# Performance work log

Measured on AMD Instinct MI355X. Metric: run time of the kernel, lower is better.

Reference implementation:

```python
import jax, jax.numpy as jnp
import numpy as np

DIM = 1024
NUM_HEADS = 16
HEAD_DIM = DIM // NUM_HEADS


def apply_rotary_embed(x, thetas):
    # x: (..., seq, d), thetas: (seq, d) broadcast over leading dims
    x1, x2 = jnp.split(x, 2, axis=-1)
    x_rot = jnp.concatenate([-x2, x1], axis=-1)
    return x * jnp.cos(thetas) + x_rot * jnp.sin(thetas)


def setup_inputs() -> dict:
    key = jax.random.key(0)
    ks = jax.random.split(key, 8)
    B, Nx, Nc = 4, 1024, 2048
    x = jax.random.normal(ks[0], (B, Nx, DIM), dtype=jnp.float32)
    c = jax.random.normal(ks[1], (B, Nc, DIM), dtype=jnp.float32)
    x_pos_embed = jax.random.normal(ks[2], (Nx, HEAD_DIM), dtype=jnp.float32)
    c_pos_embed = jax.random.normal(ks[3], (Nc, HEAD_DIM), dtype=jnp.float32)
    s = 1.0 / np.sqrt(DIM)
    Wq = jax.random.normal(ks[4], (DIM, DIM), dtype=jnp.float32) * s
    Wkv = jax.random.normal(ks[5], (DIM, 2 * DIM), dtype=jnp.float32) * s
    Wproj = jax.random.normal(ks[6], (DIM, DIM), dtype=jnp.float32) * s
    bproj = jnp.zeros((DIM,), dtype=jnp.float32)
    return {"x": x, "c": c, "x_pos_embed": x_pos_embed, "c_pos_embed": c_pos_embed,
            "Wq": Wq, "Wkv": Wkv, "Wproj": Wproj, "bproj": bproj}


def reference(x, c, x_pos_embed, c_pos_embed, Wq, Wkv, Wproj, bproj):
    B, Nx, D = x.shape
    Nc = c.shape[1]
    H, hd = NUM_HEADS, HEAD_DIM
    # Q projection -> (B, H, Nx, hd)
    q = (x @ Wq).reshape(B, Nx, H, hd).transpose(0, 2, 1, 3)
    q = apply_rotary_embed(q, x_pos_embed)
    # KV projection -> k, v each (B, H, Nc, hd)
    kv = (c @ Wkv).reshape(B, Nc, 2, H, hd).transpose(2, 0, 3, 1, 4)
    k, v = kv[0], kv[1]
    k = apply_rotary_embed(k, c_pos_embed)
    # scaled dot-product attention (dropout p=0 -> identity)
    scale = 1.0 / np.sqrt(hd).astype(np.float32)
    attn = jnp.einsum('bhqd,bhkd->bhqk', q, k) * scale
    attn = jax.nn.softmax(attn, axis=-1)
    out = jnp.einsum('bhqk,bhkd->bhqd', attn, v)
    out = out.transpose(0, 2, 1, 3).reshape(B, Nx, D)
    return out @ Wproj + bproj
```

## Files before the change

kernel.cpp:

```cpp
#include <hip/hip_runtime.h>
#include <math.h>

#define DIMC  1024
#define NHEAD 16
#define HD    64
#define NB    4
#define NX    1024
#define NC    2048
#define KD    1024

typedef _Float16 half_t;
typedef __attribute__((ext_vector_type(8))) _Float16 h8;
typedef __attribute__((ext_vector_type(4))) _Float16 h4;
typedef __attribute__((ext_vector_type(2))) __fp16 fp16x2;
typedef __attribute__((ext_vector_type(4))) float f32x4;

#define QSCALE 0.1803368801111244f
#define NEGM  -8.656170245333781f

__device__ __forceinline__ void gload_lds16(const half_t* g, half_t* l) {
    __builtin_amdgcn_global_load_lds(
        (__attribute__((address_space(1))) void*)(g),
        (__attribute__((address_space(3))) void*)(l), 16, 0, 0);
}

__device__ __forceinline__ void wtile(const float* __restrict__ W,
                                      half_t* __restrict__ Wt, int N, int IMG,
                                      int bx, int by, int t)
{
    __shared__ half_t T[64][72];
    const int k0 = by * 64, n0 = bx * 64;
    const int kr = t >> 2, c0 = (t & 3) << 4;
    const float* src = W + (size_t)(k0 + kr) * N + n0 + c0;
#pragma unroll
    for (int j = 0; j < 16; j += 4) {
        float4 v = *(const float4*)(src + j);
        T[c0 + j + 0][kr] = (half_t)v.x;
        T[c0 + j + 1][kr] = (half_t)v.y;
        T[c0 + j + 2][kr] = (half_t)v.z;
        T[c0 + j + 3][kr] = (half_t)v.w;
    }
    __syncthreads();
    const int nr = t >> 2, kc = (t & 3) << 4;
    if (!IMG) {
        half_t* dst = Wt + (size_t)(n0 + nr) * KD + k0 + kc;
        *(int4*)dst       = *(const int4*)&T[nr][kc];
        *(int4*)(dst + 8) = *(const int4*)&T[nr][kc + 8];
    } else {
        const int n = n0 + nr;
        const int ntile = n >> 8, rr = n & 255;
        const int s0 = kc >> 3;
        half_t* base = Wt + ((size_t)(ntile * 16 + by) * 256 + rr) * 64;
        *(int4*)(base + ((s0 ^ (rr & 7)) << 3))       = *(const int4*)&T[nr][kc];
        *(int4*)(base + (((s0 + 1) ^ (rr & 7)) << 3)) = *(const int4*)&T[nr][kc + 8];
    }
}

__global__ __launch_bounds__(256) void prep(
    const float* __restrict__ x, half_t* __restrict__ xh,
    const float* __restrict__ c, half_t* __restrict__ ch,
    const float* __restrict__ xpe, const float* __restrict__ cpe,
    float* __restrict__ xct, float* __restrict__ xst,
    float* __restrict__ cct, float* __restrict__ cst,
    const float* __restrict__ Wq,  half_t* __restrict__ Wqt,
    const float* __restrict__ Wkv, half_t* __restrict__ Wkt,
    const float* __restrict__ Wp,  half_t* __restrict__ Wpt)
{
    const int bid = blockIdx.x, t = threadIdx.x;
    if (bid < 1024) {
        if (bid < 256)      wtile(Wq,  Wqt, DIMC, 0,     bid & 15,         bid >> 4,         t);
        else if (bid < 768) wtile(Wkv, Wkt, 2 * DIMC, 1, (bid - 256) & 31, (bid - 256) >> 5, t);
        else                wtile(Wp,  Wpt, DIMC, 0,     (bid - 768) & 15, (bid - 768) >> 4, t);
    } else if (bid < 7168) {
        const int nx = NB * NX * DIMC;
        const int i = ((bid - 1024) * 256 + t) * 8;
        const float* s;
        h8 o;
        if (i < nx) {
            s = x + i;
            float4 a = *(const float4*)(s);
            float4 b = *(const float4*)(s + 4);
            o[0] = (half_t)a.x; o[1] = (half_t)a.y; o[2] = (half_t)a.z; o[3] = (half_t)a.w;
            o[4] = (half_t)b.x; o[5] = (half_t)b.y; o[6] = (half_t)b.z; o[7] = (half_t)b.w;
            *(h8*)(xh + i) = o;
        } else {
            const int j = i - nx;
            s = c + j;
            float4 a = *(const float4*)(s);
            float4 b = *(const float4*)(s + 4);
            o[0] = (half_t)a.x; o[1] = (half_t)a.y; o[2] = (half_t)a.z; o[3] = (half_t)a.w;
            o[4] = (half_t)b.x; o[5] = (half_t)b.y; o[6] = (half_t)b.z; o[7] = (half_t)b.w;
            const int R = j >> 10, k = j & 1023;
            const int mt = R >> 8, r = R & 255, kt = k >> 6, sl = (k & 63) >> 3;
            *(h8*)(ch + ((size_t)(mt * 16 + kt) * 256 + r) * 64 + ((sl ^ (r & 7)) << 3)) = o;
        }
    } else {
        const int i = (bid - 7168) * 256 + t;
        if (i < NX * HD) {
            const float th = xpe[i];
            xct[i] = cosf(th); xst[i] = sinf(th);
        } else {
            const int j = i - NX * HD;
            const float th = cpe[j];
            cct[j] = cosf(th); cst[j] = sinf(th);
        }
    }
}

template <int MODE, int BN>
__global__ __launch_bounds__(256) void hgemm(
    const half_t* __restrict__ Ag, const half_t* __restrict__ Bt,
    const float* __restrict__ ct, const float* __restrict__ st,
    const float* __restrict__ bias,
    void* __restrict__ out0, void* __restrict__ out1)
{
    constexpr int MI = (BN == 128) ? 4 : 2;
    constexpr int BLOADS = BN / 32;
    __shared__ half_t As[2][8192];
    __shared__ half_t Bs[2][BN * 64];

    const int tid = threadIdx.x;
    const int w = tid >> 6, lane = tid & 63;
    const int lr = lane & 15, lg = lane >> 4;
    const int wrOff = (BN == 128) ? (w >> 1) * 64 : w * 32;
    const int wcOff = (BN == 128) ? (w & 1) * 64 : 0;

    int lin = (int)blockIdx.x;
    lin = (lin & 7) * ((int)gridDim.x >> 3) + (lin >> 3);
    const int m0 = (lin >> 4) * 128, n0 = (lin & 15) * BN;

    f32x4 acc[MI][4];
#pragma unroll
    for (int i = 0; i < MI; ++i)
#pragma unroll
        for (int j = 0; j < 4; ++j) acc[i][j] = f32x4{0.f, 0.f, 0.f, 0.f};

    size_t gA[4], gB[BLOADS];
    int loff[4];
#pragma unroll
    for (int c = 0; c < 4; ++c) {
        const int L = c * 4096 + w * 1024 + lane * 16;
        const int row = L >> 7;
        const int ss = ((L >> 4) & 7) ^ (row & 7);
        gA[c] = (size_t)(m0 + row) * KD + ss * 8;
        if (c < BLOADS) gB[c] = (size_t)(n0 + row) * KD + ss * 8;
        loff[c] = c * 2048 + w * 512;
    }

#define HSTAGE(buf, kk) do {                                               \
        _Pragma("unroll")                                                  \
        for (int c = 0; c < 4; ++c) {                                      \
            gload_lds16(Ag + gA[c] + (kk) * 64, &As[buf][loff[c]]);        \
            if (c < BLOADS) gload_lds16(Bt + gB[c] + (kk) * 64, &Bs[buf][loff[c]]); \
        }                                                                  \
    } while (0)

    HSTAGE(0, 0);
    asm volatile("s_waitcnt vmcnt(0)" ::: "memory");
    __builtin_amdgcn_s_barrier();
    __builtin_amdgcn_sched_barrier(0);

    for (int k = 0; k < KD / 64; ++k) {
        const int cb = k & 1;
        if (k + 1 < KD / 64) {
            HSTAGE(cb ^ 1, k + 1);
            if constexpr (BLOADS == 4)
                asm volatile("s_waitcnt vmcnt(8)" ::: "memory");
            else
                asm volatile("s_waitcnt vmcnt(6)" ::: "memory");
        } else {
            asm volatile("s_waitcnt vmcnt(0)" ::: "memory");
        }
        __builtin_amdgcn_s_barrier();
        __builtin_amdgcn_sched_barrier(0);

        __builtin_amdgcn_s_setprio(1);
#pragma unroll
        for (int kc = 0; kc < 2; ++kc) {
            h8 af[MI], bf[4];
#pragma unroll
            for (int mi = 0; mi < MI; ++mi) {
                const int r = wrOff + mi * 16 + lr;
                af[mi] = *(const h8*)&As[cb][r * 64 + (((kc * 4 + lg) ^ (r & 7)) << 3)];
            }
#pragma unroll
            for (int ni = 0; ni < 4; ++ni) {
                const int r = wcOff + ni * 16 + lr;
                bf[ni] = *(const h8*)&Bs[cb][r * 64 + (((kc * 4 + lg) ^ (r & 7)) << 3)];
            }
#pragma unroll
            for (int mi = 0; mi < MI; ++mi)
#pragma unroll
                for (int ni = 0; ni < 4; ++ni)
                    acc[mi][ni] = __builtin_amdgcn_mfma_f32_16x16x32_f16(
                        af[mi], bf[ni], acc[mi][ni], 0, 0, 0);
        }
        __builtin_amdgcn_s_setprio(0);

        __builtin_amdgcn_s_barrier();
        __builtin_amdgcn_sched_barrier(0);
    }
#undef HSTAGE

    if (MODE == 2) {
        float* o = (float*)out0;
#pragma unroll
        for (int ni = 0; ni < 4; ++ni) {
            const int col = n0 + ni * 16 + lr;
            const float bv = bias[col];
#pragma unroll
            for (int mi = 0; mi < MI; ++mi)
#pragma unroll
                for (int r = 0; r < 4; ++r) {
                    const int row = m0 + wrOff + mi * 16 + lg * 4 + r;
                    o[(size_t)row * DIMC + col] = acc[mi][ni][r] + bv;
                }
        }
        return;
    }

    if (MODE == 0) {
        half_t* Qw = (half_t*)out0;
        const int h = n0 >> 6;
#pragma unroll
        for (int mi = 0; mi < MI; ++mi)
#pragma unroll
            for (int r = 0; r < 4; ++r) {
                const int row = m0 + wrOff + mi * 16 + lg * 4 + r;
                const int bb = row >> 10, nn = row & (NX - 1);
                const float* cr = ct + nn * HD;
                const float* sr = st + nn * HD;
                half_t* op = Qw + (((size_t)(bb * NHEAD + h)) * NX + nn) * HD;
#pragma unroll
                for (int ni = 0; ni < 4; ++ni) {
                    const int d = ni * 16 + lr;
                    const float val = acc[mi][ni][r];
                    const float pv  = acc[mi][ni ^ 2][r];
                    op[d] = (half_t)((val * cr[d] + (ni < 2 ? -pv : pv) * sr[d]) * QSCALE);
                }
            }
    }
}

__global__ __launch_bounds__(512, 2) void hgemm_kv(
    const half_t* __restrict__ Aimg, const half_t* __restrict__ Bimg,
    const float* __restrict__ ct, const float* __restrict__ st,
    half_t* __restrict__ Kw, half_t* __restrict__ Vw)
{
    __shared__ half_t lds[65536];

    const int tid = threadIdx.x;
    const int w = tid >> 6, lane = tid & 63;
    const int lr = lane & 15, lg = lane >> 4;
    const int wr = w >> 2, wc = w & 3;
    const int wrOff = wr * 128, wcOff = wc * 64;

    int lin = (int)blockIdx.x;
    lin = (lin & 7) * 32 + (lin >> 3);
    const int mt = lin >> 3, nt = lin & 7;
    const int m0 = mt * 256, n0 = nt * 256;

    const half_t* Ablk = Aimg + (size_t)mt * 262144;
    const half_t* Bblk = Bimg + (size_t)nt * 262144;
    const int so2 = w * 512 + lane * 8;

    f32x4 acc[8][4];
#pragma unroll
    for (int i = 0; i < 8; ++i)
#pragma unroll
        for (int j = 0; j < 4; ++j) acc[i][j] = f32x4{0.f, 0.f, 0.f, 0.f};
    h8 af[2][2];
    h8 bf[4][2];

#define ISSUEH(SRC, DSTOFF) do {                                     \
        gload_lds16((SRC) + so2,        &lds[(DSTOFF) + w * 512]);   \
        gload_lds16((SRC) + 4096 + so2, &lds[(DSTOFF) + 4096 + w * 512]); \
    } while (0)

#define PHASE(MI0, AOFF, BOFF, READBF, STG, GATE) do {               \
        _Pragma("unroll")                                            \
        for (int kc = 0; kc < 2; ++kc)                               \
        _Pragma("unroll")                                            \
        for (int d = 0; d < 2; ++d) {                                \
            const int r_ = wrOff + ((MI0) + d) * 16 + lr;            \
            af[d][kc] = *(const h8*)&lds[(AOFF) + r_ * 64 + (((kc * 4 + lg) ^ (r_ & 7)) << 3)]; \
        }                                                            \
        if (READBF) {                                                \
            _Pragma("unroll")                                        \
            for (int ni = 0; ni < 4; ++ni)                           \
            _Pragma("unroll")                                        \
            for (int kc = 0; kc < 2; ++kc) {                         \
                const int rb = wcOff + ni * 16 + lr;                 \
                bf[ni][kc] = *(const h8*)&lds[(BOFF) + rb * 64 + (((kc * 4 + lg) ^ (rb & 7)) << 3)]; \
            }                                                        \
        }                                                            \
        STG;                                                         \
        __builtin_amdgcn_sched_barrier(0);                           \
        __builtin_amdgcn_s_barrier();                                \
        __builtin_amdgcn_s_setprio(1);                               \
        _Pragma("unroll")                                            \
        for (int d = 0; d < 2; ++d)                                  \
        _Pragma("unroll")                                            \
        for (int ni = 0; ni < 4; ++ni)                               \
        _Pragma("unroll")                                            \
        for (int kc = 0; kc < 2; ++kc)                               \
            acc[(MI0) + d][ni] = __builtin_amdgcn_mfma_f32_16x16x32_f16( \
                af[d][kc], bf[ni][kc], acc[(MI0) + d][ni], 0, 0, 0); \
        __builtin_amdgcn_s_setprio(0);                               \
        GATE;                                                        \
        __builtin_amdgcn_s_barrier();                                \
    } while (0)

#define GATE4 asm volatile("s_waitcnt vmcnt(4)" ::: "memory")
#define GATE0 asm volatile("s_waitcnt vmcnt(0)" ::: "memory")
#define NOG   ((void)0)

    ISSUEH(Ablk, 0);          ISSUEH(Ablk + 8192, 8192);
    ISSUEH(Bblk, 32768);      ISSUEH(Bblk + 8192, 32768 + 8192);
    __builtin_amdgcn_sched_barrier(0);
    ISSUEH(Bblk + 16384, 49152); ISSUEH(Bblk + 16384 + 8192, 49152 + 8192);
    asm volatile("s_waitcnt vmcnt(4)" ::: "memory");
    __builtin_amdgcn_s_barrier();

    for (int i = 0; i < 7; ++i) {
        const half_t* An1 = Ablk + (size_t)(2 * i + 1) * 16384;
        const half_t* An2 = Ablk + (size_t)(2 * i + 2) * 16384;
        const half_t* Bn2 = Bblk + (size_t)(2 * i + 2) * 16384;
        const half_t* Bn3 = Bblk + (size_t)(2 * i + 3) * 16384;
        PHASE(0, 0,     32768, true,  ISSUEH(An1, 16384),               NOG);
        PHASE(2, 0,     32768, false, ISSUEH(An1 + 8192, 16384 + 8192), NOG);
        PHASE(4, 0,     32768, false, ISSUEH(Bn2, 32768),               NOG);
        PHASE(6, 0,     32768, false, ISSUEH(Bn2 + 8192, 32768 + 8192), GATE4);
        PHASE(0, 16384, 49152, true,  ISSUEH(An2, 0),                   NOG);
        PHASE(2, 16384, 49152, false, ISSUEH(An2 + 8192, 8192),         NOG);
        PHASE(4, 16384, 49152, false, ISSUEH(Bn3, 49152),               NOG);
        PHASE(6, 16384, 49152, false, ISSUEH(Bn3 + 8192, 49152 + 8192), GATE4);
    }
    {
        const half_t* A15 = Ablk + (size_t)15 * 16384;
        PHASE(0, 0,     32768, true,  ISSUEH(A15, 16384),               NOG);
        PHASE(2, 0,     32768, false, ISSUEH(A15 + 8192, 16384 + 8192), NOG);
        PHASE(4, 0,     32768, false, NOG,                              NOG);
        PHASE(6, 0,     32768, false, NOG,                              GATE0);
        PHASE(0, 16384, 49152, true,  NOG,                              NOG);
        PHASE(2, 16384, 49152, false, NOG,                              NOG);
        PHASE(4, 16384, 49152, false, NOG,                              NOG);
        PHASE(6, 16384, 49152, false, NOG,                              NOG);
    }
#undef PHASE
#undef ISSUEH
#undef GATE4
#undef GATE0
#undef NOG

    const bool isK = (n0 < DIMC);
    const int h = ((n0 & (DIMC - 1)) >> 6) + wc;
#pragma unroll
    for (int mi = 0; mi < 8; ++mi)
#pragma unroll
        for (int r = 0; r < 4; ++r) {
            const int row = m0 + wrOff + mi * 16 + lg * 4 + r;
            const int bb = row >> 11, nn = row & (NC - 1);
            const int tt = nn >> 6, rr = nn & 63;
            const size_t tbase = ((size_t)(bb * NHEAD + h) * 32 + tt) * 4096;
            const float* cr = ct + nn * HD;
            const float* sr = st + nn * HD;
#pragma unroll
            for (int ni = 0; ni < 4; ++ni) {
                const int d = ni * 16 + lr;
                const float val = acc[mi][ni][r];
                if (isK) {
                    const float pv = acc[mi][ni ^ 2][r];
                    Kw[tbase + rr * 64 + ((((d >> 3) ^ (rr & 7)) << 3) | (d & 7))] =
                        (half_t)(val * cr[d] + (ni < 2 ? -pv : pv) * sr[d]);
                } else {
                    Vw[tbase + d * 64 + ((((rr >> 3) ^ (d & 7)) << 3) | (rr & 7))] =
                        (half_t)val;
                }
            }
        }
}

__global__ __launch_bounds__(256) void attn_mfma(
    const half_t* __restrict__ Q, const half_t* __restrict__ Kg,
    const half_t* __restrict__ Vg,
    float* __restrict__ Opart, float* __restrict__ Lpart)
{
    __shared__ half_t Ks[2][4096];
    __shared__ half_t Vs[2][4096];
    __shared__ half_t Ps[8192];

    const int tid = threadIdx.x;
    const int w = tid >> 6, lane = tid & 63;
    const int lr = lane & 15, lg = lane >> 4;
    const int e7 = lr & 7;

    const int inner = (int)blockIdx.x & 511;
    const int kvh = (int)blockIdx.x >> 9;
    const int sid = (inner & 7) * 64 + (inner >> 3);
    const int bh = sid >> 3;
    const int q0 = (sid & 7) * 128;

    const half_t* qbase = Q + ((size_t)bh * NX + q0 + w * 16 + lr) * HD + lg * 8;
    const h8 qf0a = *(const h8*)(qbase);
    const h8 qf1a = *(const h8*)(qbase + 32);
    const h8 qf0b = *(const h8*)(qbase + (size_t)64 * HD);
    const h8 qf1b = *(const h8*)(qbase + (size_t)64 * HD + 32);

    f32x4 acc[2][4];
#pragma unroll
    for (int qb = 0; qb < 2; ++qb)
#pragma unroll
        for (int i = 0; i < 4; ++i) acc[qb][i] = f32x4{0.f, 0.f, 0.f, 0.f};
    f32x4 accl[2] = {{0.f, 0.f, 0.f, 0.f}, {0.f, 0.f, 0.f, 0.f}};

    h8 vone;
#pragma unroll
    for (int i = 0; i < 8; ++i) vone[i] = (half_t)(lr == 0 ? 1.0f : 0.0f);

    const half_t* Kt = Kg + (size_t)bh * 32 * 4096;
    const half_t* Vt = Vg + (size_t)bh * 32 * 4096;
    const int so = w * 512 + lane * 8;
    const int t0 = kvh * 16, t1 = t0 + 16;

#define STAGE(bi, t) do {                                           \
        const half_t* kg_ = Kt + (size_t)(t) * 4096;                \
        const half_t* vg_ = Vt + (size_t)(t) * 4096;                \
        gload_lds16(kg_ + so,        &Ks[bi][w * 512]);             \
        gload_lds16(kg_ + 2048 + so, &Ks[bi][2048 + w * 512]);      \
        gload_lds16(vg_ + so,        &Vs[bi][w * 512]);             \
        gload_lds16(vg_ + 2048 + so, &Vs[bi][2048 + w * 512]);      \
    } while (0)

    STAGE(0, t0);
    asm volatile("s_waitcnt vmcnt(0)" ::: "memory");
    __builtin_amdgcn_s_barrier();
    __builtin_amdgcn_sched_barrier(0);

    const int rowq = w * 16 + lr;

    for (int t = t0; t < t1; ++t) {
        const int cur = t & 1;
        if (t + 1 < t1) {
            STAGE(cur ^ 1, t + 1);
            asm volatile("s_waitcnt vmcnt(4)" ::: "memory");
        } else {
            asm volatile("s_waitcnt vmcnt(0)" ::: "memory");
        }
        __builtin_amdgcn_s_barrier();
        __builtin_amdgcn_sched_barrier(0);

        h8 kfr[4][2];
#pragma unroll
        for (int cb = 0; cb < 4; ++cb) {
            const int r = cb * 16 + lr;
            kfr[cb][0] = *(const h8*)&Ks[cur][r * 64 + ((lg ^ e7) << 3)];
            kfr[cb][1] = *(const h8*)&Ks[cur][r * 64 + (((4 + lg) ^ e7) << 3)];
        }

#pragma unroll
        for (int qb = 0; qb < 2; ++qb) {
            const h8 q0f = qb ? qf0b : qf0a;
            const h8 q1f = qb ? qf1b : qf1a;
            const int rowp = qb * 64 + rowq;

            f32x4 sc[4];
            __builtin_amdgcn_s_setprio(1);
#pragma unroll
            for (int cb = 0; cb < 4; ++cb) {
                f32x4 a = {NEGM, NEGM, NEGM, NEGM};
                a = __builtin_amdgcn_mfma_f32_16x16x32_f16(kfr[cb][0], q0f, a, 0, 0, 0);
                a = __builtin_amdgcn_mfma_f32_16x16x32_f16(kfr[cb][1], q1f, a, 0, 0, 0);
                sc[cb] = a;
            }
            __builtin_amdgcn_s_setprio(0);

#pragma unroll
            for (int cb = 0; cb < 4; ++cb) {
                fp16x2 a01 = __builtin_amdgcn_cvt_pkrtz(exp2f(sc[cb][0]), exp2f(sc[cb][1]));
                fp16x2 a23 = __builtin_amdgcn_cvt_pkrtz(exp2f(sc[cb][2]), exp2f(sc[cb][3]));
                union { h4 h; uint2 u; } pw;
                pw.u.x = *(unsigned int*)&a01;
                pw.u.y = *(unsigned int*)&a23;
                const int s = cb * 2 + (lg >> 1);
                *(h4*)&Ps[rowp * 64 + ((s ^ e7) << 3) + (lg & 1) * 4] = pw.h;
            }
        }

        h8 pf[2][2];
#pragma unroll
        for (int qb = 0; qb < 2; ++qb) {
            const int rowp = qb * 64 + rowq;
            pf[qb][0] = *(const h8*)&Ps[rowp * 64 + ((lg ^ e7) << 3)];
            pf[qb][1] = *(const h8*)&Ps[rowp * 64 + (((4 + lg) ^ e7) << 3)];
        }

        __builtin_amdgcn_s_setprio(1);
#pragma unroll
        for (int db = 0; db < 4; ++db) {
            const int rd = db * 16 + lr;
            const h8 vf0 = *(const h8*)&Vs[cur][rd * 64 + ((lg ^ e7) << 3)];
            const h8 vf1 = *(const h8*)&Vs[cur][rd * 64 + (((4 + lg) ^ e7) << 3)];
#pragma unroll
            for (int qb = 0; qb < 2; ++qb) {
                acc[qb][db] = __builtin_amdgcn_mfma_f32_16x16x32_f16(pf[qb][0], vf0, acc[qb][db], 0, 0, 0);
                acc[qb][db] = __builtin_amdgcn_mfma_f32_16x16x32_f16(pf[qb][1], vf1, acc[qb][db], 0, 0, 0);
            }
        }
#pragma unroll
        for (int qb = 0; qb < 2; ++qb) {
            accl[qb] = __builtin_amdgcn_mfma_f32_16x16x32_f16(pf[qb][0], vone, accl[qb], 0, 0, 0);
            accl[qb] = __builtin_amdgcn_mfma_f32_16x16x32_f16(pf[qb][1], vone, accl[qb], 0, 0, 0);
        }
        __builtin_amdgcn_s_setprio(0);

        __builtin_amdgcn_s_barrier();
        __builtin_amdgcn_sched_barrier(0);
    }
#undef STAGE

#pragma unroll
    for (int qb = 0; qb < 2; ++qb) {
        const int qblk = (q0 >> 6) + qb;
        const int slot = (bh * 16 + qblk) * 2 + kvh;
        float* Po = Opart + (size_t)slot * 4096;
#pragma unroll
        for (int db = 0; db < 4; ++db)
#pragma unroll
            for (int r = 0; r < 4; ++r)
                Po[(w * 16 + lg * 4 + r) * 64 + db * 16 + lr] = acc[qb][db][r];
        if (lr == 0) {
#pragma unroll
            for (int r = 0; r < 4; ++r)
                Lpart[(size_t)slot * 64 + w * 16 + lg * 4 + r] = accl[qb][r];
        }
    }
}

__global__ __launch_bounds__(256) void combine(
    const float* __restrict__ Opart, const float* __restrict__ Lpart,
    half_t* __restrict__ Ow)
{
    const int pidx = blockIdx.x;
    const int bh = pidx >> 4, qblk = pidx & 15;
    const int b = bh >> 4, h = bh & 15;
    const int t = threadIdx.x;
    const int row = t >> 2;
    const int c0 = (t & 3) << 4;

    const float* P0 = Opart + (size_t)(pidx * 2 + 0) * 4096 + row * 64 + c0;
    const float* P1 = Opart + (size_t)(pidx * 2 + 1) * 4096 + row * 64 + c0;
    const float inv = 1.f / (Lpart[(size_t)(pidx * 2 + 0) * 64 + row] +
                             Lpart[(size_t)(pidx * 2 + 1) * 64 + row]);

    half_t* o = Ow + ((size_t)b * NX + qblk * 64 + row) * DIMC + h * 64 + c0;
#pragma unroll
    for (int j = 0; j < 16; j += 8) {
        float4 a0 = *(const float4*)(P0 + j);
        float4 a1 = *(const float4*)(P0 + j + 4);
        float4 b0 = *(const float4*)(P1 + j);
        float4 b1 = *(const float4*)(P1 + j + 4);
        h8 ov;
        ov[0] = (half_t)((a0.x + b0.x) * inv);
        ov[1] = (half_t)((a0.y + b0.y) * inv);
        ov[2] = (half_t)((a0.z + b0.z) * inv);
        ov[3] = (half_t)((a0.w + b0.w) * inv);
        ov[4] = (half_t)((a1.x + b1.x) * inv);
        ov[5] = (half_t)((a1.y + b1.y) * inv);
        ov[6] = (half_t)((a1.z + b1.z) * inv);
        ov[7] = (half_t)((a1.w + b1.w) * inv);
        *(h8*)(o + j) = ov;
    }
}

extern "C" void kernel_launch(void* const* d_in, const int* in_sizes, int n_in,
                              void* d_out, int out_size, void* d_ws, size_t ws_size,
                              hipStream_t stream)
{
    const float* x     = (const float*)d_in[0];
    const float* c     = (const float*)d_in[1];
    const float* xpe   = (const float*)d_in[2];
    const float* cpe   = (const float*)d_in[3];
    const float* Wq    = (const float*)d_in[4];
    const float* Wkv   = (const float*)d_in[5];
    const float* Wproj = (const float*)d_in[6];
    const float* bproj = (const float*)d_in[7];

    char* wsb = (char*)d_ws;
    half_t* xh  = (half_t*)(wsb);
    half_t* ch  = (half_t*)(wsb + ((size_t)8  << 20));
    half_t* Wqt = (half_t*)(wsb + ((size_t)24 << 20));
    half_t* Wkt = (half_t*)(wsb + ((size_t)26 << 20));
    half_t* Kw  = (half_t*)(wsb + ((size_t)32 << 20));
    half_t* Vw  = (half_t*)(wsb + ((size_t)48 << 20));
    half_t* Ow  = (half_t*)(wsb + ((size_t)64 << 20));
    float*  xct = (float*)(wsb + ((size_t)72 << 20));
    float*  xst = (float*)(wsb + ((size_t)72 << 20) + (256u << 10));
    float*  cct = (float*)(wsb + ((size_t)72 << 20) + (512u << 10));
    float*  cst = (float*)(wsb + ((size_t)72 << 20) + (1024u << 10));
    half_t* Wpt = (half_t*)(wsb + ((size_t)74 << 20));
    float*  Lpart = (float*)(wsb + ((size_t)76 << 20));
    float*  Opart = (float*)(wsb);
    half_t* Qw  = (half_t*)d_out;

    prep<<<7936, 256, 0, stream>>>(x, xh, c, ch, xpe, cpe,
                                   xct, xst, cct, cst,
                                   Wq, Wqt, Wkv, Wkt, Wproj, Wpt);

    hgemm<0, 64><<<512, 256, 0, stream>>>(xh, Wqt, xct, xst, nullptr,
                                          Qw, nullptr);
    hgemm_kv<<<256, 512, 0, stream>>>(ch, Wkt, cct, cst, Kw, Vw);
    attn_mfma<<<1024, 256, 0, stream>>>(Qw, Kw, Vw, Opart, Lpart);
    combine<<<1024, 256, 0, stream>>>(Opart, Lpart, Ow);
    hgemm<2, 64><<<512, 256, 0, stream>>>(Ow, Wpt, nullptr, nullptr, bproj,
                                          (float*)d_out, nullptr);
}
```

Measured before the change: 184.3 us.

## Fuse split-KV combine into the output projection GEMM A-tile load

Removes the separate combine kernel and the fp16 Ow intermediate. The projection GEMM now reads the two fp32 partial attention outputs and their softmax denominators, sums and normalizes them in registers, converts to fp16 and writes the result into swizzled LDS as the A operand. This saves one launch and a round trip of Ow through global memory. In exchange each GEMM block re-reads fp32 partials (twice the bytes of the fp16 data), and the 16 column blocks per row tile each read them again, which raises global traffic and register pressure.

```diff
diff --git a/kernel.cpp b/kernel.cpp
--- a/kernel.cpp
+++ b/kernel.cpp
@@ -202,23 +202,6 @@
     }
 #undef HSTAGE
 
-    if (MODE == 2) {
-        float* o = (float*)out0;
-#pragma unroll
-        for (int ni = 0; ni < 4; ++ni) {
-            const int col = n0 + ni * 16 + lr;
-            const float bv = bias[col];
-#pragma unroll
-            for (int mi = 0; mi < MI; ++mi)
-#pragma unroll
-                for (int r = 0; r < 4; ++r) {
-                    const int row = m0 + wrOff + mi * 16 + lg * 4 + r;
-                    o[(size_t)row * DIMC + col] = acc[mi][ni][r] + bv;
-                }
-        }
-        return;
-    }
-
     if (MODE == 0) {
         half_t* Qw = (half_t*)out0;
         const int h = n0 >> 6;
@@ -537,39 +520,145 @@
     }
 }
 
-__global__ __launch_bounds__(256) void combine(
+__global__ __launch_bounds__(256) void hgemm_proj(
     const float* __restrict__ Opart, const float* __restrict__ Lpart,
-    half_t* __restrict__ Ow)
+    const half_t* __restrict__ Bt, const float* __restrict__ bias,
+    float* __restrict__ out)
 {
-    const int pidx = blockIdx.x;
-    const int bh = pidx >> 4, qblk = pidx & 15;
-    const int b = bh >> 4, h = bh & 15;
-    const int t = threadIdx.x;
-    const int row = t >> 2;
-    const int c0 = (t & 3) << 4;
-
-    const float* P0 = Opart + (size_t)(pidx * 2 + 0) * 4096 + row * 64 + c0;
-    const float* P1 = Opart + (size_t)(pidx * 2 + 1) * 4096 + row * 64 + c0;
-    const float inv = 1.f / (Lpart[(size_t)(pidx * 2 + 0) * 64 + row] +
-                             Lpart[(size_t)(pidx * 2 + 1) * 64 + row]);
-
-    half_t* o = Ow + ((size_t)b * NX + qblk * 64 + row) * DIMC + h * 64 + c0;
-#pragma unroll
-    for (int j = 0; j < 16; j += 8) {
-        float4 a0 = *(const float4*)(P0 + j);
-        float4 a1 = *(const float4*)(P0 + j + 4);
-        float4 b0 = *(const float4*)(P1 + j);
-        float4 b1 = *(const float4*)(P1 + j + 4);
-        h8 ov;
-        ov[0] = (half_t)((a0.x + b0.x) * inv);
-        ov[1] = (half_t)((a0.y + b0.y) * inv);
-        ov[2] = (half_t)((a0.z + b0.z) * inv);
-        ov[3] = (half_t)((a0.w + b0.w) * inv);
-        ov[4] = (half_t)((a1.x + b1.x) * inv);
-        ov[5] = (half_t)((a1.y + b1.y) * inv);
-        ov[6] = (half_t)((a1.z + b1.z) * inv);
-        ov[7] = (half_t)((a1.w + b1.w) * inv);
-        *(h8*)(o + j) = ov;
+    __shared__ half_t As[2][8192];
+    __shared__ half_t Bs[2][4096];
+
+    const int tid = threadIdx.x;
+    const int w = tid >> 6, lane = tid & 63;
+    const int lr = lane & 15, lg = lane >> 4;
+    const int wrOff = w * 32;
+
+    int lin = (int)blockIdx.x;
+    lin = (lin & 7) * 64 + (lin >> 3);
+    const int m0 = (lin >> 4) * 128, n0 = (lin & 15) * 64;
+
+    f32x4 acc[2][4];
+#pragma unroll
+    for (int i = 0; i < 2; ++i)
+#pragma unroll
+        for (int j = 0; j < 4; ++j) acc[i][j] = f32x4{0.f, 0.f, 0.f, 0.f};
+
+    const int arow = tid >> 1;
+    const int d0 = (tid & 1) * 32;
+    const int am = m0 + arow;
+    const int ab = am >> 10, an = am & (NX - 1);
+    const int aq = an >> 6, arIn = an & 63;
+
+    size_t gB[2];
+    int loff[2];
+#pragma unroll
+    for (int c = 0; c < 2; ++c) {
+        const int L = c * 4096 + w * 1024 + lane * 16;
+        const int row = L >> 7;
+        const int ss = ((L >> 4) & 7) ^ (row & 7);
+        gB[c] = (size_t)(n0 + row) * KD + ss * 8;
+        loff[c] = c * 2048 + w * 512;
+    }
+
+    float4 ra[8], rb[8];
+    float linv;
+
+#define ALOAD(kk) do {                                                      \
+        const int pidx_ = ((ab * NHEAD + (kk)) * 16 + aq);                  \
+        const float* P0_ = Opart + (size_t)pidx_ * 8192 + arIn * 64 + d0;   \
+        const float* P1_ = P0_ + 4096;                                      \
+        _Pragma("unroll")                                                   \
+        for (int j = 0; j < 4; ++j) {                                       \
+            ra[j]     = *(const float4*)(P0_ + j * 8);                      \
+            ra[j + 4] = *(const float4*)(P0_ + j * 8 + 4);                  \
+            rb[j]     = *(const float4*)(P1_ + j * 8);                      \
+            rb[j + 4] = *(const float4*)(P1_ + j * 8 + 4);                  \
+        }                                                                   \
+        linv = 1.f / (Lpart[(size_t)pidx_ * 128 + arIn] +                   \
+                      Lpart[(size_t)pidx_ * 128 + 64 + arIn]);              \
+    } while (0)
+
+#define AWRITE(buf) do {                                                    \
+        _Pragma("unroll")                                                   \
+        for (int j = 0; j < 4; ++j) {                                       \
+            float4 s0 = ra[j], s1 = rb[j], s2 = ra[j + 4], s3 = rb[j + 4];  \
+            fp16x2 c0_ = __builtin_amdgcn_cvt_pkrtz((s0.x + s1.x) * linv,   \
+                                                    (s0.y + s1.y) * linv);  \
+            fp16x2 c1_ = __builtin_amdgcn_cvt_pkrtz((s0.z + s1.z) * linv,   \
+                                                    (s0.w + s1.w) * linv);  \
+            fp16x2 c2_ = __builtin_amdgcn_cvt_pkrtz((s2.x + s3.x) * linv,   \
+                                                    (s2.y + s3.y) * linv);  \
+            fp16x2 c3_ = __builtin_amdgcn_cvt_pkrtz((s2.z + s3.z) * linv,   \
+                                                    (s2.w + s3.w) * linv);  \
+            union { h8 h; unsigned int u[4]; } pk;                          \
+            pk.u[0] = *(unsigned int*)&c0_; pk.u[1] = *(unsigned int*)&c1_; \
+            pk.u[2] = *(unsigned int*)&c2_; pk.u[3] = *(unsigned int*)&c3_; \
+            const int sl = ((d0 >> 3) + j) ^ (arow & 7);                    \
+            *(h8*)&As[buf][arow * 64 + sl * 8] = pk.h;                      \
+        }                                                                   \
+    } while (0)
+
+    ALOAD(0);
+    gload_lds16(Bt + gB[0], &Bs[0][loff[0]]);
+    gload_lds16(Bt + gB[1], &Bs[0][loff[1]]);
+    asm volatile("s_waitcnt vmcnt(0)" ::: "memory");
+    AWRITE(0);
+    __syncthreads();
+
+    for (int k = 0; k < 16; ++k) {
+        const int cb = k & 1;
+
+        h8 af[2], bf[4];
+#pragma unroll
+        for (int kc = 0; kc < 2; ++kc) { (void)kc; }
+        if (k + 1 < 16) {
+            ALOAD(k + 1);
+            gload_lds16(Bt + gB[0] + (k + 1) * 64, &Bs[cb ^ 1][loff[0]]);
+            gload_lds16(Bt + gB[1] + (k + 1) * 64, &Bs[cb ^ 1][loff[1]]);
+        }
+
+        __builtin_amdgcn_s_setprio(1);
+#pragma unroll
+        for (int kc = 0; kc < 2; ++kc) {
+#pragma unroll
+            for (int mi = 0; mi < 2; ++mi) {
+                const int r = wrOff + mi * 16 + lr;
+                af[mi] = *(const h8*)&As[cb][r * 64 + (((kc * 4 + lg) ^ (r & 7)) << 3)];
+            }
+#pragma unroll
+            for (int ni = 0; ni < 4; ++ni) {
+                const int r = ni * 16 + lr;
+                bf[ni] = *(const h8*)&Bs[cb][r * 64 + (((kc * 4 + lg) ^ (r & 7)) << 3)];
+            }
+#pragma unroll
+            for (int mi = 0; mi < 2; ++mi)
+#pragma unroll
+                for (int ni = 0; ni < 4; ++ni)
+                    acc[mi][ni] = __builtin_amdgcn_mfma_f32_16x16x32_f16(
+                        af[mi], bf[ni], acc[mi][ni], 0, 0, 0);
+        }
+        __builtin_amdgcn_s_setprio(0);
+
+        if (k + 1 < 16) {
+            asm volatile("s_waitcnt vmcnt(0)" ::: "memory");
+            AWRITE(cb ^ 1);
+        }
+        __syncthreads();
+    }
+#undef ALOAD
+#undef AWRITE
+
+#pragma unroll
+    for (int ni = 0; ni < 4; ++ni) {
+        const int col = n0 + ni * 16 + lr;
+        const float bv = bias[col];
+#pragma unroll
+        for (int mi = 0; mi < 2; ++mi)
+#pragma unroll
+            for (int r = 0; r < 4; ++r) {
+                const int row = m0 + wrOff + mi * 16 + lg * 4 + r;
+                out[(size_t)row * DIMC + col] = acc[mi][ni][r] + bv;
+            }
     }
 }
 
@@ -593,7 +682,6 @@
     half_t* Wkt = (half_t*)(wsb + ((size_t)26 << 20));
     half_t* Kw  = (half_t*)(wsb + ((size_t)32 << 20));
     half_t* Vw  = (half_t*)(wsb + ((size_t)48 << 20));
-    half_t* Ow  = (half_t*)(wsb + ((size_t)64 << 20));
     float*  xct = (float*)(wsb + ((size_t)72 << 20));
     float*  xst = (float*)(wsb + ((size_t)72 << 20) + (256u << 10));
     float*  cct = (float*)(wsb + ((size_t)72 << 20) + (512u << 10));
@@ -611,7 +699,6 @@
                                           Qw, nullptr);
     hgemm_kv<<<256, 512, 0, stream>>>(ch, Wkt, cct, cst, Kw, Vw);
     attn_mfma<<<1024, 256, 0, stream>>>(Qw, Kw, Vw, Opart, Lpart);
-    combine<<<1024, 256, 0, stream>>>(Opart, Lpart, Ow);
-    hgemm<2, 64><<<512, 256, 0, stream>>>(Ow, Wpt, nullptr, nullptr, bproj,
-                                          (float*)d_out, nullptr);
+    hgemm_proj<<<512, 256, 0, stream>>>(Opart, Lpart, Wpt, bproj,
+                                        (float*)d_out);
 }
```

After: 232.0 us. 1.26x slower.
